# Performance work log

Hardware: AMD Instinct MI355X
Metric: run time of the kernel (lower is better)

Reference implementation:

```python
import jax, jax.numpy as jnp
import numpy as np

V = 196608      # HEALPix nside=128 vertices
DEG = 9         # nnz per row (8 neighbors + self)
C = 64          # in_channels == out_channels
K = 8           # Chebyshev kernel_size
B = 1
EPS = 1e-5


def setup_inputs() -> dict:
    key = jax.random.key(0)
    ks = jax.random.split(key, 8)
    nnz = V * DEG
    x = jax.random.normal(ks[0], (B, V, C), dtype=jnp.float32)
    lap_rows = jnp.repeat(jnp.arange(V, dtype=jnp.int64), DEG)
    lap_cols = jax.random.randint(ks[1], (nnz,), 0, V, dtype=jnp.int64)
    lap_vals = jax.random.normal(ks[2], (nnz,), dtype=jnp.float32) * 0.1
    gamma = jnp.ones((C,), dtype=jnp.float32)
    beta = jnp.zeros((C,), dtype=jnp.float32)
    # Chebyshev weight [K, Fin, Fout], kaiming-like scale
    weight = jax.random.normal(ks[3], (K, C, C), dtype=jnp.float32) * (1.0 / np.sqrt(C * K))
    bias = jnp.zeros((C,), dtype=jnp.float32)
    return {"x": x, "lap_rows": lap_rows, "lap_cols": lap_cols, "lap_vals": lap_vals,
            "gamma": gamma, "beta": beta, "weight": weight, "bias": bias}


def _mish(h):
    return h * jnp.tanh(jax.nn.softplus(h))


def reference(x, lap_rows, lap_cols, lap_vals, gamma, beta, weight, bias):
    Bb, Vv, Cc = x.shape
    Kk = weight.shape[0]
    # BatchNorm1d (training-mode batch stats) over (B, V) per channel
    mean = jnp.mean(x, axis=(0, 1))
    var = jnp.var(x, axis=(0, 1))
    h = (x - mean) * jax.lax.rsqrt(var + EPS) * gamma + beta
    # Mish activation
    h = _mish(h)
    # Chebyshev spectral conv: x_k = 2*L@x_{k-1} - x_{k-2}
    def lap_mm(y):  # y: [V, M] sparse L @ y via gather + segment-sum scatter
        return jax.ops.segment_sum(lap_vals[:, None] * y[lap_cols], lap_rows,
                                   num_segments=Vv)
    x0 = jnp.transpose(h, (1, 0, 2)).reshape(Vv, Bb * Cc)  # [V, B*Fin]
    xs = [x0]
    if Kk > 1:
        xs.append(lap_mm(x0))
    for _ in range(2, Kk):
        xs.append(2.0 * lap_mm(xs[-1]) - xs[-2])
    Xk = jnp.stack(xs, axis=0).reshape(Kk, Vv, Bb, Cc)  # [K, V, B, Fin]
    out = jnp.einsum('kvbi,kio->bvo', Xk, weight) + bias  # [B, V, Fout]
    return out
```

## Files before the change

### kernel.cpp

```cpp
#include <hip/hip_runtime.h>
#include <math.h>

#define NV 196608
#define NDEG 9
#define NC 64
#define NK 8
#define TILE 64
#define NBLK (NV / TILE)
#define SLOT ((size_t)NV * NC)
static constexpr float EPS = 1e-5f;

typedef __attribute__((ext_vector_type(8))) short bf16x8;
typedef __attribute__((ext_vector_type(4))) short bf16x4;
typedef __attribute__((ext_vector_type(4))) float f32x4;
typedef int   i32x4u __attribute__((ext_vector_type(4), aligned(4)));
typedef float f32x4u __attribute__((ext_vector_type(4), aligned(4)));

__device__ __forceinline__ short f2bf(float f) {
    unsigned u = __float_as_uint(f);
    unsigned r = (u + 0x7fffu + ((u >> 16) & 1u)) >> 16;
    return (short)r;
}
__device__ __forceinline__ float bf2f(short h) {
    return __uint_as_float(((unsigned)(unsigned short)h) << 16);
}

__device__ __forceinline__ float mish_f(float h) {
    float t = __expf(fminf(h, 20.f));
    float p = 1.f + t;
    float p2 = p * p;
    return h * ((p2 - 1.f) / (p2 + 1.f));
}

__global__ void __launch_bounds__(256) stats_wconv_kernel(
    const float* __restrict__ x, float* __restrict__ stats,
    const float* __restrict__ w, unsigned short* __restrict__ Wb) {
    if (blockIdx.x >= 1024) {
        int idx = (blockIdx.x - 1024) * 256 + threadIdx.x;
        int i = idx & 63, o = (idx >> 6) & 63, k = idx >> 12;
        Wb[idx] = (unsigned short)f2bf(w[k * 4096 + i * 64 + o]);
        return;
    }
    const float4* x4 = (const float4*)x;
    int t = blockIdx.x * 256 + threadIdx.x;
    int stride = 1024 * 256;
    float4 s = {0.f, 0.f, 0.f, 0.f}, ss = {0.f, 0.f, 0.f, 0.f};
    for (int i = t; i < NV * (NC / 4); i += stride) {
        float4 v = x4[i];
        s.x += v.x; s.y += v.y; s.z += v.z; s.w += v.w;
        ss.x += v.x * v.x; ss.y += v.y * v.y; ss.z += v.z * v.z; ss.w += v.w * v.w;
    }
    __shared__ float4 ls[256], lss[256];
    ls[threadIdx.x] = s;
    lss[threadIdx.x] = ss;
    __syncthreads();
    if (threadIdx.x < 64) {
        int ch = threadIdx.x;
        int g = ch >> 2, comp = ch & 3;
        float a = 0.f, b = 0.f;
        #pragma unroll
        for (int k = 0; k < 16; ++k) {
            float4 v1 = ls[k * 16 + g];
            float4 v2 = lss[k * 16 + g];
            a += (comp == 0) ? v1.x : (comp == 1) ? v1.y : (comp == 2) ? v1.z : v1.w;
            b += (comp == 0) ? v2.x : (comp == 1) ? v2.y : (comp == 2) ? v2.z : v2.w;
        }
        atomicAdd(&stats[ch], a);
        atomicAdd(&stats[64 + ch], b);
    }
}

__global__ void __launch_bounds__(256) bn_mish_k0(
    const float* __restrict__ x, const float* __restrict__ stats,
    const float* __restrict__ gamma, const float* __restrict__ beta,
    unsigned short* __restrict__ dst) {
    int lane = threadIdx.x & 63;
    int wave = threadIdx.x >> 6;
    int c4 = lane & 15, rg = lane >> 4;
    int tile0 = blockIdx.x * TILE;

    float4 sc, sh;
    {
        float4 su = ((const float4*)stats)[c4];
        float4 sq = ((const float4*)stats)[16 + c4];
        float4 g4 = ((const float4*)gamma)[c4];
        float4 b4 = ((const float4*)beta)[c4];
        #define BNC(comp) { float mu = su.comp * (1.f / NV);                     \
                            float va = sq.comp * (1.f / NV) - mu * mu;           \
                            float rs = rsqrtf(va + EPS);                         \
                            sc.comp = g4.comp * rs;                              \
                            sh.comp = b4.comp - mu * sc.comp; }
        BNC(x) BNC(y) BNC(z) BNC(w)
        #undef BNC
    }

    const float4* x4 = (const float4*)x;
    #pragma unroll
    for (int it = 0; it < 4; ++it) {
        int v = tile0 + wave * 16 + it * 4 + rg;
        float4 h = x4[v * 16 + c4];
        float4 m;
        m.x = mish_f(h.x * sc.x + sh.x);
        m.y = mish_f(h.y * sc.y + sh.y);
        m.z = mish_f(h.z * sc.z + sh.z);
        m.w = mish_f(h.w * sc.w + sh.w);
        bf16x4 xb = { f2bf(m.x), f2bf(m.y), f2bf(m.z), f2bf(m.w) };
        *(bf16x4*)(dst + (size_t)v * NC + 4 * c4) = xb;
    }
}

template <bool FIRST>
__global__ void __launch_bounds__(256) cheb_step(
    const int* __restrict__ cols, const float* __restrict__ vals,
    const unsigned short* __restrict__ src, const unsigned short* __restrict__ prev,
    unsigned short* __restrict__ dst) {
    int lane = threadIdx.x & 63;
    int wave = threadIdx.x >> 6;
    int c8 = lane & 7, rg = lane >> 3;
    int tile0 = blockIdx.x * TILE;

    #pragma unroll
    for (int it = 0; it < 2; ++it) {
        int v = tile0 + wave * 16 + it * 8 + rg;
        const int* cp = cols + v * NDEG;
        const float* vp = vals + v * NDEG;
        i32x4u c03 = __builtin_nontemporal_load((const i32x4u*)cp);
        i32x4u c47 = __builtin_nontemporal_load((const i32x4u*)(cp + 4));
        int    cl8 = __builtin_nontemporal_load(cp + 8);
        f32x4u a03 = __builtin_nontemporal_load((const f32x4u*)vp);
        f32x4u a47 = __builtin_nontemporal_load((const f32x4u*)(vp + 4));
        float  al8 = __builtin_nontemporal_load(vp + 8);

        int   cj[NDEG] = { c03[0], c03[1], c03[2], c03[3],
                           c47[0], c47[1], c47[2], c47[3], cl8 };
        float aj[NDEG] = { a03[0], a03[1], a03[2], a03[3],
                           a47[0], a47[1], a47[2], a47[3], al8 };

        bf16x8 g[NDEG];
        #pragma unroll
        for (int j = 0; j < NDEG; ++j)
            g[j] = *(const bf16x8*)(src + (size_t)cj[j] * NC + c8 * 8);

        float s[8] = {0.f, 0.f, 0.f, 0.f, 0.f, 0.f, 0.f, 0.f};
        #pragma unroll
        for (int j = 0; j < NDEG; ++j)
            #pragma unroll
            for (int q = 0; q < 8; ++q) s[q] += aj[j] * bf2f(g[j][q]);

        bf16x8 xb;
        if (FIRST) {
            #pragma unroll
            for (int q = 0; q < 8; ++q) xb[q] = f2bf(s[q]);
        } else {
            bf16x8 p = __builtin_nontemporal_load(
                           (const bf16x8*)(prev + (size_t)v * NC + c8 * 8));
            #pragma unroll
            for (int q = 0; q < 8; ++q) xb[q] = f2bf(2.f * s[q] - bf2f(p[q]));
        }
        __builtin_nontemporal_store(xb, (bf16x8*)(dst + (size_t)v * NC + c8 * 8));
    }
}

__global__ void __launch_bounds__(256) gemm_all(
    const unsigned short* __restrict__ basis, const unsigned short* __restrict__ Wb,
    const float* __restrict__ bias, float* __restrict__ out) {
    __shared__ short Wl[NK * NC * NC];
    __shared__ short At[2][4][1024];

    const int tid  = threadIdx.x;
    const int lane = tid & 63;
    const int wave = tid >> 6;
    const int m16  = lane & 15, qq = lane >> 4;
    const int tile0 = blockIdx.x * TILE;

    #pragma unroll
    for (int h = 0; h < 16; ++h) {
        int ci = tid + h * 256;
        int k = ci >> 9, o = (ci >> 3) & 63, c = ci & 7;
        bf16x8 w = *(const bf16x8*)(Wb + (size_t)ci * 8);
        *(bf16x8*)&Wl[k * 4096 + o * 64 + ((c ^ (o & 7)) * 8)] = w;
    }
    __syncthreads();

    const int r0 = lane >> 3;
    const int cc = lane & 7;
    const unsigned short* abase = basis + (size_t)(tile0 + wave * 16) * NC;
    short* mybuf0 = &At[0][wave][0];
    short* mybuf1 = &At[1][wave][0];

    #define ALOAD(dst0, dst1, k_)                                                  \
        { const unsigned short* p = abase + (size_t)(k_) * SLOT;                   \
          dst0 = __builtin_nontemporal_load((const bf16x8*)(p + r0 * 64 + cc * 8));\
          dst1 = __builtin_nontemporal_load((const bf16x8*)(p + (r0 + 8) * 64 + cc * 8)); }
    #define AWRITE(buf, s0, s1)                                                    \
        { *(bf16x8*)&buf[r0 * 64 + ((cc ^ (r0 & 7)) * 8)] = s0;                    \
          *(bf16x8*)&buf[(r0 + 8) * 64 + ((cc ^ ((r0 + 8) & 7)) * 8)] = s1; }

    bf16x8 p00, p01, p10, p11;
    ALOAD(p00, p01, 0)
    ALOAD(p10, p11, 1)
    AWRITE(mybuf0, p00, p01)

    f32x4 acc[4];
    #pragma unroll
    for (int nt = 0; nt < 4; ++nt) acc[nt] = (f32x4){0.f, 0.f, 0.f, 0.f};

    #pragma unroll
    for (int k = 0; k < NK; ++k) {
        if (k + 2 < NK) {
            if ((k & 1) == 0) { ALOAD(p00, p01, k + 2) }
            else              { ALOAD(p10, p11, k + 2) }
        }
        const short* ab = (k & 1) ? mybuf1 : mybuf0;
        bf16x8 a0 = *(const bf16x8*)&ab[m16 * 64 + ((qq ^ (m16 & 7)) * 8)];
        bf16x8 a1 = *(const bf16x8*)&ab[m16 * 64 + (((qq + 4) ^ (m16 & 7)) * 8)];
        const short* wk = &Wl[k * 4096];
        #pragma unroll
        for (int nt = 0; nt < 4; ++nt) {
            int o = nt * 16 + m16;
            bf16x8 b0 = *(const bf16x8*)&wk[o * 64 + ((qq ^ (o & 7)) * 8)];
            bf16x8 b1 = *(const bf16x8*)&wk[o * 64 + (((qq + 4) ^ (o & 7)) * 8)];
            acc[nt] = __builtin_amdgcn_mfma_f32_16x16x32_bf16(a0, b0, acc[nt], 0, 0, 0);
            acc[nt] = __builtin_amdgcn_mfma_f32_16x16x32_bf16(a1, b1, acc[nt], 0, 0, 0);
        }
        if (k + 1 < NK) {
            short* nb = (k & 1) ? mybuf0 : mybuf1;
            if ((k & 1) == 0) { AWRITE(nb, p10, p11) }
            else              { AWRITE(nb, p00, p01) }
        }
    }
    #undef ALOAD
    #undef AWRITE

    #pragma unroll
    for (int nt = 0; nt < 4; ++nt) {
        float bcol = bias[nt * 16 + m16];
        #pragma unroll
        for (int r = 0; r < 4; ++r) {
            int vout = tile0 + wave * 16 + qq * 4 + r;
            out[(size_t)vout * NC + nt * 16 + m16] = acc[nt][r] + bcol;
        }
    }
}

__global__ void __launch_bounds__(256) gemm_bases(
    const unsigned short* __restrict__ basis, const unsigned short* __restrict__ Wb,
    const float* __restrict__ bias, float* __restrict__ out,
    int kb, int kc, int S, int first) {
    int lane = threadIdx.x & 63;
    int wave = threadIdx.x >> 6;
    int m16 = lane & 15, qq = lane >> 4;
    int tile0 = blockIdx.x * TILE;

    f32x4 acc[4];
    #pragma unroll
    for (int nt = 0; nt < 4; ++nt) acc[nt] = (f32x4){0.f, 0.f, 0.f, 0.f};

    #pragma unroll 1
    for (int j = 0; j < kc; ++j) {
        int k = kb + j;
        const unsigned short* bs =
            basis + (size_t)(k % S) * SLOT + (size_t)(tile0 + wave * 16 + m16) * NC;
        bf16x8 a0 = __builtin_nontemporal_load((const bf16x8*)(bs + qq * 8));
        bf16x8 a1 = __builtin_nontemporal_load((const bf16x8*)(bs + 32 + qq * 8));
        const unsigned short* wk = Wb + (size_t)k * NC * NC;
        #pragma unroll
        for (int nt = 0; nt < 4; ++nt) {
            const unsigned short* wr = wk + (nt * 16 + m16) * NC;
            bf16x8 b0 = *(const bf16x8*)(wr + qq * 8);
            bf16x8 b1 = *(const bf16x8*)(wr + 32 + qq * 8);
            acc[nt] = __builtin_amdgcn_mfma_f32_16x16x32_bf16(a0, b0, acc[nt], 0, 0, 0);
            acc[nt] = __builtin_amdgcn_mfma_f32_16x16x32_bf16(a1, b1, acc[nt], 0, 0, 0);
        }
    }

    #pragma unroll
    for (int nt = 0; nt < 4; ++nt) {
        float bcol = bias[nt * 16 + m16];
        #pragma unroll
        for (int r = 0; r < 4; ++r) {
            int vout = tile0 + wave * 16 + qq * 4 + r;
            float* po = out + (size_t)vout * NC + nt * 16 + m16;
            *po = first ? (acc[nt][r] + bcol) : (*po + acc[nt][r]);
        }
    }
}

extern "C" void kernel_launch(void* const* d_in, const int* in_sizes, int n_in,
                              void* d_out, int out_size, void* d_ws, size_t ws_size,
                              hipStream_t stream) {
    const float* x      = (const float*)d_in[0];
    const int*   cols   = (const int*)  d_in[2];
    const float* vals   = (const float*)d_in[3];
    const float* gamma  = (const float*)d_in[4];
    const float* beta   = (const float*)d_in[5];
    const float* weight = (const float*)d_in[6];
    const float* bias   = (const float*)d_in[7];
    float* out = (float*)d_out;

    char* wsb = (char*)d_ws;
    float*          stats = (float*)wsb;
    unsigned short* Wb    = (unsigned short*)(wsb + 1024);
    unsigned short* basis = (unsigned short*)(wsb + 131072);

    int S = (int)((ws_size - 131072) / (SLOT * sizeof(unsigned short)));
    if (S > NK) S = NK;
    if (S < 3) S = 3;

    hipMemsetAsync(stats, 0, 1024, stream);
    stats_wconv_kernel<<<1152, 256, 0, stream>>>(x, stats, weight, Wb);
    bn_mish_k0<<<NBLK, 256, 0, stream>>>(x, stats, gamma, beta, basis);

    if (S >= NK) {
        for (int k = 1; k < NK; ++k) {
            const unsigned short* src = basis + (size_t)(k - 1) * SLOT;
            unsigned short*       dst = basis + (size_t)k * SLOT;
            if (k == 1) {
                cheb_step<true><<<NBLK, 256, 0, stream>>>(cols, vals, src, src, dst);
            } else {
                const unsigned short* prev = basis + (size_t)(k - 2) * SLOT;
                cheb_step<false><<<NBLK, 256, 0, stream>>>(cols, vals, src, prev, dst);
            }
        }
        gemm_all<<<NBLK, 256, 0, stream>>>(basis, Wb, bias, out);
    } else {
        int kb = 0, gsize = S, first = 1;
        while (kb < NK) {
            int kc = (gsize < NK - kb) ? gsize : (NK - kb);
            for (int k = (kb == 0 ? 1 : kb); k < kb + kc; ++k) {
                const unsigned short* src = basis + (size_t)((k - 1) % S) * SLOT;
                unsigned short*       dst = basis + (size_t)(k % S) * SLOT;
                if (k == 1) {
                    cheb_step<true><<<NBLK, 256, 0, stream>>>(cols, vals, src, src, dst);
                } else {
                    const unsigned short* prev = basis + (size_t)((k - 2) % S) * SLOT;
                    cheb_step<false><<<NBLK, 256, 0, stream>>>(cols, vals, src, prev, dst);
                }
            }
            gemm_bases<<<NBLK, 256, 0, stream>>>(basis, Wb, bias, out, kb, kc, S, first);
            first = 0;
            kb += kc;
            gsize = S - 2;
        }
    }
}
```

Baseline: 468.0 us.

## Stream per-k weight slices through double-buffered LDS in gemm_all; drop nontemporal hints

gemm_all no longer preloads all 8 weight slices into 64KB of LDS. It now double-buffers one basis tile and one weight slice per k, with block-wide syncs between steps. This cuts LDS use and should allow more resident blocks, at the cost of a __syncthreads per k step. Separately, the nontemporal loads and stores in cheb_step and gemm_bases become plain accesses, so L2 can cache the gathered rows and outputs.

```diff
diff --git a/kernel.cpp b/kernel.cpp
--- a/kernel.cpp
+++ b/kernel.cpp
@@ -31,6 +31,8 @@
     float p2 = p * p;
     return h * ((p2 - 1.f) / (p2 + 1.f));
 }
+
+#define LDSOFF(r, c) ((r) * 64 + (((c) ^ ((r) & 7)) * 8))
 
 __global__ void __launch_bounds__(256) stats_wconv_kernel(
     const float* __restrict__ x, float* __restrict__ stats,
@@ -124,12 +126,12 @@
         int v = tile0 + wave * 16 + it * 8 + rg;
         const int* cp = cols + v * NDEG;
         const float* vp = vals + v * NDEG;
-        i32x4u c03 = __builtin_nontemporal_load((const i32x4u*)cp);
-        i32x4u c47 = __builtin_nontemporal_load((const i32x4u*)(cp + 4));
-        int    cl8 = __builtin_nontemporal_load(cp + 8);
-        f32x4u a03 = __builtin_nontemporal_load((const f32x4u*)vp);
-        f32x4u a47 = __builtin_nontemporal_load((const f32x4u*)(vp + 4));
-        float  al8 = __builtin_nontemporal_load(vp + 8);
+        i32x4u c03 = *(const i32x4u*)cp;
+        i32x4u c47 = *(const i32x4u*)(cp + 4);
+        int    cl8 = cp[8];
+        f32x4u a03 = *(const f32x4u*)vp;
+        f32x4u a47 = *(const f32x4u*)(vp + 4);
+        float  al8 = vp[8];
 
         int   cj[NDEG] = { c03[0], c03[1], c03[2], c03[3],
                            c47[0], c47[1], c47[2], c47[3], cl8 };
@@ -157,15 +159,15 @@
             #pragma unroll
             for (int q = 0; q < 8; ++q) xb[q] = f2bf(2.f * s[q] - bf2f(p[q]));
         }
-        __builtin_nontemporal_store(xb, (bf16x8*)(dst + (size_t)v * NC + c8 * 8));
+        *(bf16x8*)(dst + (size_t)v * NC + c8 * 8) = xb;
     }
 }
 
 __global__ void __launch_bounds__(256) gemm_all(
     const unsigned short* __restrict__ basis, const unsigned short* __restrict__ Wb,
     const float* __restrict__ bias, float* __restrict__ out) {
-    __shared__ short Wl[NK * NC * NC];
-    __shared__ short At[2][4][1024];
+    __shared__ short Al[2][NC * NC];
+    __shared__ short Wl[2][NC * NC];
 
     const int tid  = threadIdx.x;
     const int lane = tid & 63;
@@ -173,64 +175,59 @@
     const int m16  = lane & 15, qq = lane >> 4;
     const int tile0 = blockIdx.x * TILE;
 
-    #pragma unroll
-    for (int h = 0; h < 16; ++h) {
-        int ci = tid + h * 256;
-        int k = ci >> 9, o = (ci >> 3) & 63, c = ci & 7;
-        bf16x8 w = *(const bf16x8*)(Wb + (size_t)ci * 8);
-        *(bf16x8*)&Wl[k * 4096 + o * 64 + ((c ^ (o & 7)) * 8)] = w;
+    const int rA = tid >> 3, cA = tid & 7;
+
+    bf16x8 pa0, pa1, pw0, pw1;
+    {
+        const unsigned short* bp = basis + (size_t)(tile0 + rA) * NC + cA * 8;
+        pa0 = __builtin_nontemporal_load((const bf16x8*)bp);
+        pa1 = __builtin_nontemporal_load((const bf16x8*)(bp + 32 * NC));
+        pw0 = *(const bf16x8*)(Wb + rA * NC + cA * 8);
+        pw1 = *(const bf16x8*)(Wb + (rA + 32) * NC + cA * 8);
+        *(bf16x8*)&Al[0][LDSOFF(rA, cA)] = pa0;
+        *(bf16x8*)&Al[0][LDSOFF(rA + 32, cA)] = pa1;
+        *(bf16x8*)&Wl[0][LDSOFF(rA, cA)] = pw0;
+        *(bf16x8*)&Wl[0][LDSOFF(rA + 32, cA)] = pw1;
     }
     __syncthreads();
 
-    const int r0 = lane >> 3;
-    const int cc = lane & 7;
-    const unsigned short* abase = basis + (size_t)(tile0 + wave * 16) * NC;
-    short* mybuf0 = &At[0][wave][0];
-    short* mybuf1 = &At[1][wave][0];
-
-    #define ALOAD(dst0, dst1, k_)                                                  \
-        { const unsigned short* p = abase + (size_t)(k_) * SLOT;                   \
-          dst0 = __builtin_nontemporal_load((const bf16x8*)(p + r0 * 64 + cc * 8));\
-          dst1 = __builtin_nontemporal_load((const bf16x8*)(p + (r0 + 8) * 64 + cc * 8)); }
-    #define AWRITE(buf, s0, s1)                                                    \
-        { *(bf16x8*)&buf[r0 * 64 + ((cc ^ (r0 & 7)) * 8)] = s0;                    \
-          *(bf16x8*)&buf[(r0 + 8) * 64 + ((cc ^ ((r0 + 8) & 7)) * 8)] = s1; }
-
-    bf16x8 p00, p01, p10, p11;
-    ALOAD(p00, p01, 0)
-    ALOAD(p10, p11, 1)
-    AWRITE(mybuf0, p00, p01)
-
     f32x4 acc[4];
     #pragma unroll
     for (int nt = 0; nt < 4; ++nt) acc[nt] = (f32x4){0.f, 0.f, 0.f, 0.f};
 
     #pragma unroll
     for (int k = 0; k < NK; ++k) {
-        if (k + 2 < NK) {
-            if ((k & 1) == 0) { ALOAD(p00, p01, k + 2) }
-            else              { ALOAD(p10, p11, k + 2) }
-        }
-        const short* ab = (k & 1) ? mybuf1 : mybuf0;
-        bf16x8 a0 = *(const bf16x8*)&ab[m16 * 64 + ((qq ^ (m16 & 7)) * 8)];
-        bf16x8 a1 = *(const bf16x8*)&ab[m16 * 64 + (((qq + 4) ^ (m16 & 7)) * 8)];
-        const short* wk = &Wl[k * 4096];
+        if (k + 1 < NK) {
+            const unsigned short* bp =
+                basis + (size_t)(k + 1) * SLOT + (size_t)(tile0 + rA) * NC + cA * 8;
+            pa0 = __builtin_nontemporal_load((const bf16x8*)bp);
+            pa1 = __builtin_nontemporal_load((const bf16x8*)(bp + 32 * NC));
+            const unsigned short* wp = Wb + (k + 1) * NC * NC;
+            pw0 = *(const bf16x8*)(wp + rA * NC + cA * 8);
+            pw1 = *(const bf16x8*)(wp + (rA + 32) * NC + cA * 8);
+        }
+        const short* ab = Al[k & 1];
+        const short* wb = Wl[k & 1];
+        bf16x8 a0 = *(const bf16x8*)&ab[LDSOFF(wave * 16 + m16, qq)];
+        bf16x8 a1 = *(const bf16x8*)&ab[LDSOFF(wave * 16 + m16, qq + 4)];
         #pragma unroll
         for (int nt = 0; nt < 4; ++nt) {
             int o = nt * 16 + m16;
-            bf16x8 b0 = *(const bf16x8*)&wk[o * 64 + ((qq ^ (o & 7)) * 8)];
-            bf16x8 b1 = *(const bf16x8*)&wk[o * 64 + (((qq + 4) ^ (o & 7)) * 8)];
+            bf16x8 b0 = *(const bf16x8*)&wb[LDSOFF(o, qq)];
+            bf16x8 b1 = *(const bf16x8*)&wb[LDSOFF(o, qq + 4)];
             acc[nt] = __builtin_amdgcn_mfma_f32_16x16x32_bf16(a0, b0, acc[nt], 0, 0, 0);
             acc[nt] = __builtin_amdgcn_mfma_f32_16x16x32_bf16(a1, b1, acc[nt], 0, 0, 0);
         }
         if (k + 1 < NK) {
-            short* nb = (k & 1) ? mybuf0 : mybuf1;
-            if ((k & 1) == 0) { AWRITE(nb, p10, p11) }
-            else              { AWRITE(nb, p00, p01) }
-        }
-    }
-    #undef ALOAD
-    #undef AWRITE
+            short* an = Al[(k + 1) & 1];
+            short* wn = Wl[(k + 1) & 1];
+            *(bf16x8*)&an[LDSOFF(rA, cA)] = pa0;
+            *(bf16x8*)&an[LDSOFF(rA + 32, cA)] = pa1;
+            *(bf16x8*)&wn[LDSOFF(rA, cA)] = pw0;
+            *(bf16x8*)&wn[LDSOFF(rA + 32, cA)] = pw1;
+            __syncthreads();
+        }
+    }
 
     #pragma unroll
     for (int nt = 0; nt < 4; ++nt) {
@@ -261,8 +258,8 @@
         int k = kb + j;
         const unsigned short* bs =
             basis + (size_t)(k % S) * SLOT + (size_t)(tile0 + wave * 16 + m16) * NC;
-        bf16x8 a0 = __builtin_nontemporal_load((const bf16x8*)(bs + qq * 8));
-        bf16x8 a1 = __builtin_nontemporal_load((const bf16x8*)(bs + 32 + qq * 8));
+        bf16x8 a0 = *(const bf16x8*)(bs + qq * 8);
+        bf16x8 a1 = *(const bf16x8*)(bs + 32 + qq * 8);
         const unsigned short* wk = Wb + (size_t)k * NC * NC;
         #pragma unroll
         for (int nt = 0; nt < 4; ++nt) {
```

After: 446.8 us. -4.5%, faster.
